# Performance work log

Measured on AMD Instinct MI355X. Metric: run time of the kernel, lower is better.

The kernel has to match this reference:

```python
import jax, jax.numpy as jnp
import numpy as np

EPS = 1e-4
MAX_LAPLACE_VAR = 1000.0
MAX_DENSITY = 10000.0
BINS = 256

_LAP_KERNEL = jnp.array([[0., 1., 0.], [1., -4., 1.], [0., 1., 0.]], dtype=jnp.float32)[None, None]  # OIHW [1,1,3,3]


def setup_inputs() -> dict:
    key = jax.random.key(0)
    k1, k2 = jax.random.split(key)
    rgb_img = jax.random.uniform(k1, (32, 3, 512, 512), dtype=jnp.float32)
    depth_img = jax.random.normal(k2, (32, 1, 512, 512), dtype=jnp.float32)
    return {"rgb_img": rgb_img, "depth_img": depth_img}


def _rgb_confidence(rgb_img):
    B, C, H, W = rgb_img.shape
    gray = 0.299 * rgb_img[:, 0] + 0.587 * rgb_img[:, 1] + 0.114 * rgb_img[:, 2]  # [B,H,W]
    gray = gray[:, None]  # [B,1,H,W]
    lap = jax.lax.conv_general_dilated(
        gray, _LAP_KERNEL, window_strides=(1, 1), padding=[(1, 1), (1, 1)],
        dimension_numbers=("NCHW", "OIHW", "NCHW"))
    # torch.var default is unbiased (ddof=1)
    laplace_var = jnp.var(lap, axis=(1, 2, 3), ddof=1)

    # integer-valued pixels 0..255 land exactly in histc bins 0..255 (bins=256, min=0, max=255)
    vals = jnp.clip(gray * 255.0, 0.0, 255.0).astype(jnp.int32)  # [B,1,H,W]
    vals = vals.reshape(B, -1)  # [B, H*W]
    bidx = jnp.broadcast_to(jnp.arange(B)[:, None], vals.shape)
    hist = jnp.zeros((B, BINS), jnp.float32).at[bidx, vals].add(1.0)
    p = hist / jnp.sum(hist, axis=1, keepdims=True)
    entropy = -jnp.sum(p * jnp.log2(p + EPS), axis=1)

    clarity_score = laplace_var / (MAX_LAPLACE_VAR + EPS)
    uniformity_score = 1.0 / (entropy + EPS)
    return (0.5 * (clarity_score + uniformity_score))[:, None]  # [B,1]


def _depth_confidence(depth_img):
    C = depth_img.shape[1]
    depth_map = depth_img[:, 2] if C == 3 else depth_img[:, 0]  # [B,H,W]
    mask = (depth_map > 0).astype(jnp.float32)
    density = jnp.mean(mask, axis=(1, 2))

    # vectorized masked std (unbiased, ddof=1), matching torch.std over valid pixels
    n = jnp.sum(mask, axis=(1, 2))  # [B]
    mean = jnp.sum(depth_map * mask, axis=(1, 2)) / jnp.maximum(n, 1.0)
    sq = jnp.sum(mask * (depth_map - mean[:, None, None]) ** 2, axis=(1, 2))
    var = sq / jnp.maximum(n - 1.0, 1.0)
    std = jnp.sqrt(jnp.maximum(var, 0.0))
    noise_level = jnp.where(n > 0, std, 1.0)

    density_score = density / (MAX_DENSITY + EPS)
    noise_score = 1.0 / (noise_level + EPS)
    return (0.5 * (density_score + noise_score))[:, None]  # [B,1]


def reference(rgb_img, depth_img):
    rgb_conf = _rgb_confidence(rgb_img)
    depth_conf = _depth_confidence(depth_img)
    denom = rgb_conf + depth_conf + EPS
    w_r = rgb_conf / denom
    w_d = depth_conf / denom
    return (w_r, w_d)
```

## Files before the change

### kernel.cpp

```cpp
#include <hip/hip_runtime.h>

#define IMG_H 512
#define IMG_W 512
#define HW (IMG_H * IMG_W)
#define NB 32
#define STRIPS 64
#define RPW 2

#define ACCP_DOUBLES (5 * NB * STRIPS)
#define HISTP_U32 (NB * STRIPS * 256)
#define WS_BYTES (ACCP_DOUBLES * 8 + HISTP_U32 * 4)

struct Row6 { float4 a0, a1, b0, b1, c0, c1; };

__device__ inline Row6 load_row(const float* __restrict__ rp, int r, int c0) {
    Row6 x;
    if ((unsigned)r < IMG_H) {
        const size_t o = (size_t)r * IMG_W + c0;
        x.a0 = *(const float4*)(rp + o);
        x.a1 = *(const float4*)(rp + o + 4);
        x.b0 = *(const float4*)(rp + HW + o);
        x.b1 = *(const float4*)(rp + HW + o + 4);
        x.c0 = *(const float4*)(rp + 2 * HW + o);
        x.c1 = *(const float4*)(rp + 2 * HW + o + 4);
    } else {
        const float4 z = {0.f, 0.f, 0.f, 0.f};
        x.a0 = x.a1 = x.b0 = x.b1 = x.c0 = x.c1 = z;
    }
    return x;
}

__device__ inline void to_gray(const Row6& x, float g[8]) {
    g[0] = 0.299f * x.a0.x + 0.587f * x.b0.x + 0.114f * x.c0.x;
    g[1] = 0.299f * x.a0.y + 0.587f * x.b0.y + 0.114f * x.c0.y;
    g[2] = 0.299f * x.a0.z + 0.587f * x.b0.z + 0.114f * x.c0.z;
    g[3] = 0.299f * x.a0.w + 0.587f * x.b0.w + 0.114f * x.c0.w;
    g[4] = 0.299f * x.a1.x + 0.587f * x.b1.x + 0.114f * x.c1.x;
    g[5] = 0.299f * x.a1.y + 0.587f * x.b1.y + 0.114f * x.c1.y;
    g[6] = 0.299f * x.a1.z + 0.587f * x.b1.z + 0.114f * x.c1.z;
    g[7] = 0.299f * x.a1.w + 0.587f * x.b1.w + 0.114f * x.c1.w;
}

__global__ __launch_bounds__(256, 2) void fused_kernel(
    const float* __restrict__ rgb, const float* __restrict__ depth,
    double* __restrict__ accp, unsigned int* __restrict__ histp)
{
    __shared__ unsigned int lh[4][256];
    __shared__ double red[4][5];

    const int t = threadIdx.x;
    const int b = blockIdx.y;
    const int x = blockIdx.x;
    const int s = ((x & 7) << 3) | (x >> 3);
    const int lane = t & 63;
    const int w = t >> 6;

    #pragma unroll
    for (int i = 0; i < 4; ++i) lh[i][t] = 0u;
    __syncthreads();

    const float* rp = rgb + (size_t)b * 3 * HW;
    const int rb = s * (4 * RPW) + w * RPW;
    const int c0 = lane * 8;

    const float4* dp = (const float4*)(depth + (size_t)b * HW + (size_t)s * (HW / STRIPS));

    Row6 r0 = load_row(rp, rb - 1, c0);
    Row6 r1 = load_row(rp, rb, c0);
    Row6 buf[2];
    float4 dv[2][2];
    buf[0] = load_row(rp, rb + 1, c0); dv[0][0] = dp[0 * 256 + t]; dv[0][1] = dp[1 * 256 + t];
    buf[1] = load_row(rp, rb + 2, c0); dv[1][0] = dp[2 * 256 + t]; dv[1][1] = dp[3 * 256 + t];

    float gp[8], gc[8], gn[8];
    to_gray(r0, gp);
    to_gray(r1, gc);

    float s1 = 0.f, s2 = 0.f;
    float dnf = 0.f, dsf = 0.f, dqf = 0.f;

    #pragma unroll
    for (int r = 0; r < RPW; ++r) {
        to_gray(buf[r], gn);
        const float4 d0 = dv[r][0];
        const float4 d1 = dv[r][1];

        float lf = __shfl_up(gc[7], 1, 64);
        if (lane == 0) lf = 0.f;
        float rt = __shfl_down(gc[0], 1, 64);
        if (lane == 63) rt = 0.f;

        #pragma unroll
        for (int j = 0; j < 8; ++j) {
            const float left  = (j == 0) ? lf : gc[j - 1];
            const float right = (j == 7) ? rt : gc[j + 1];
            const float lap = gp[j] + gn[j] + left + right - 4.f * gc[j];
            s1 += lap;
            s2 += lap * lap;
            atomicAdd(&lh[w][(int)fminf(fmaxf(gc[j] * 255.f, 0.f), 255.f)], 1u);
        }

        if (d0.x > 0.f) { dnf += 1.f; dsf += d0.x; dqf += d0.x * d0.x; }
        if (d0.y > 0.f) { dnf += 1.f; dsf += d0.y; dqf += d0.y * d0.y; }
        if (d0.z > 0.f) { dnf += 1.f; dsf += d0.z; dqf += d0.z * d0.z; }
        if (d0.w > 0.f) { dnf += 1.f; dsf += d0.w; dqf += d0.w * d0.w; }
        if (d1.x > 0.f) { dnf += 1.f; dsf += d1.x; dqf += d1.x * d1.x; }
        if (d1.y > 0.f) { dnf += 1.f; dsf += d1.y; dqf += d1.y * d1.y; }
        if (d1.z > 0.f) { dnf += 1.f; dsf += d1.z; dqf += d1.z * d1.z; }
        if (d1.w > 0.f) { dnf += 1.f; dsf += d1.w; dqf += d1.w * d1.w; }

        #pragma unroll
        for (int j = 0; j < 8; ++j) { gp[j] = gc[j]; gc[j] = gn[j]; }
    }

    double z0 = (double)s1, z1 = (double)s2, z2 = (double)dnf, z3 = (double)dsf, z4 = (double)dqf;
    for (int off = 32; off > 0; off >>= 1) {
        z0 += __shfl_down(z0, off, 64);
        z1 += __shfl_down(z1, off, 64);
        z2 += __shfl_down(z2, off, 64);
        z3 += __shfl_down(z3, off, 64);
        z4 += __shfl_down(z4, off, 64);
    }
    if (lane == 0) {
        red[w][0] = z0; red[w][1] = z1; red[w][2] = z2; red[w][3] = z3; red[w][4] = z4;
    }
    __syncthreads();

    const unsigned int hsum = lh[0][t] + lh[1][t] + lh[2][t] + lh[3][t];
    histp[((size_t)b * STRIPS + s) * 256 + t] = hsum;
    if (t < 5) {
        const double v = red[0][t] + red[1][t] + red[2][t] + red[3][t];
        accp[((size_t)t * NB + b) * STRIPS + s] = v;
    }
}

__global__ __launch_bounds__(256) void final_kernel(
    const double* __restrict__ accp,
    const unsigned int* __restrict__ histp,
    float* __restrict__ out)
{
    __shared__ float ent[4];
    __shared__ double sacc[5];

    const int t = threadIdx.x;
    const int b = blockIdx.x;
    const int lane = t & 63;
    const int w = t >> 6;

    unsigned int hv = 0u;
    #pragma unroll
    for (int s = 0; s < STRIPS; ++s)
        hv += histp[((size_t)b * STRIPS + s) * 256 + t];

    const float p = (float)hv * (1.0f / (float)HW);
    float term = p * log2f(p + 1e-4f);
    for (int off = 32; off > 0; off >>= 1) term += __shfl_down(term, off, 64);
    if (lane == 0) ent[w] = term;

    if (t < 160) {
        const int k = t >> 5, ss = t & 31;
        double v = accp[((size_t)k * NB + b) * STRIPS + ss]
                 + accp[((size_t)k * NB + b) * STRIPS + ss + 32];
        for (int off = 16; off > 0; off >>= 1) v += __shfl_down(v, off, 32);
        if (ss == 0) sacc[k] = v;
    }
    __syncthreads();

    if (t == 0) {
        const double entropy = -(double)(ent[0] + ent[1] + ent[2] + ent[3]);
        const double N = (double)HW;

        const double ls = sacc[0], lq = sacc[1];
        const double lvar = (lq - ls * ls / N) / (N - 1.0);
        const double clarity = lvar / (1000.0 + 1e-4);
        const double uniformity = 1.0 / (entropy + 1e-4);
        const double rgb_conf = 0.5 * (clarity + uniformity);

        const double n = sacc[2], sdep = sacc[3], q = sacc[4];
        const double mean = sdep / fmax(n, 1.0);
        const double sq = q - 2.0 * mean * sdep + mean * mean * n;
        const double var = sq / fmax(n - 1.0, 1.0);
        const double stdd = sqrt(fmax(var, 0.0));
        const double noise = (n > 0.0) ? stdd : 1.0;
        const double density = n / N;
        const double depth_conf = 0.5 * (density / (10000.0 + 1e-4) + 1.0 / (noise + 1e-4));

        const double denom = rgb_conf + depth_conf + 1e-4;
        out[b]      = (float)(rgb_conf / denom);
        out[NB + b] = (float)(depth_conf / denom);
    }
}

extern "C" void kernel_launch(void* const* d_in, const int* in_sizes, int n_in,
                              void* d_out, int out_size, void* d_ws, size_t ws_size,
                              hipStream_t stream) {
    const float* rgb   = (const float*)d_in[0];
    const float* depth = (const float*)d_in[1];
    float* out = (float*)d_out;

    double* accp = (double*)d_ws;
    unsigned int* histp = (unsigned int*)((char*)d_ws + ACCP_DOUBLES * 8);

    fused_kernel<<<dim3(STRIPS, NB), 256, 0, stream>>>(rgb, depth, accp, histp);
    final_kernel<<<NB, 256, 0, stream>>>(accp, histp, out);
}
```

Measured before the change: 173.6 us.

## Split rows into column halves with deeper per-warp row streaming

Each block now covers half the image width (4 floats per lane) over 4 rows per warp instead of full width over 2 rows. Halo columns at the split are fetched with scalar edge loads. Row loads are software-pipelined one row ahead instead of all up front, which cuts register pressure, and launch bounds rise to 4 blocks per CU for more occupancy. The cost is extra scalar edge loads and smaller 16-byte accesses per lane, and the previous strip swizzle is dropped.

```diff
diff --git a/kernel.cpp b/kernel.cpp
--- a/kernel.cpp
+++ b/kernel.cpp
@@ -4,44 +4,46 @@
 #define IMG_W 512
 #define HW (IMG_H * IMG_W)
 #define NB 32
-#define STRIPS 64
-#define RPW 2
-
-#define ACCP_DOUBLES (5 * NB * STRIPS)
-#define HISTP_U32 (NB * STRIPS * 256)
+#define NSX 64
+#define RPW 4
+#define DSLOT (HW / NSX)
+
+#define ACCP_DOUBLES (5 * NB * NSX)
+#define HISTP_U32 (NB * NSX * 256)
 #define WS_BYTES (ACCP_DOUBLES * 8 + HISTP_U32 * 4)
 
-struct Row6 { float4 a0, a1, b0, b1, c0, c1; };
-
-__device__ inline Row6 load_row(const float* __restrict__ rp, int r, int c0) {
-    Row6 x;
+struct RowH { float4 a, b, c; };
+
+__device__ inline RowH load_rowh(const float* __restrict__ rp, int r, int c0) {
+    RowH x;
     if ((unsigned)r < IMG_H) {
         const size_t o = (size_t)r * IMG_W + c0;
-        x.a0 = *(const float4*)(rp + o);
-        x.a1 = *(const float4*)(rp + o + 4);
-        x.b0 = *(const float4*)(rp + HW + o);
-        x.b1 = *(const float4*)(rp + HW + o + 4);
-        x.c0 = *(const float4*)(rp + 2 * HW + o);
-        x.c1 = *(const float4*)(rp + 2 * HW + o + 4);
+        x.a = *(const float4*)(rp + o);
+        x.b = *(const float4*)(rp + HW + o);
+        x.c = *(const float4*)(rp + 2 * HW + o);
     } else {
         const float4 z = {0.f, 0.f, 0.f, 0.f};
-        x.a0 = x.a1 = x.b0 = x.b1 = x.c0 = x.c1 = z;
+        x.a = x.b = x.c = z;
     }
     return x;
 }
 
-__device__ inline void to_gray(const Row6& x, float g[8]) {
-    g[0] = 0.299f * x.a0.x + 0.587f * x.b0.x + 0.114f * x.c0.x;
-    g[1] = 0.299f * x.a0.y + 0.587f * x.b0.y + 0.114f * x.c0.y;
-    g[2] = 0.299f * x.a0.z + 0.587f * x.b0.z + 0.114f * x.c0.z;
-    g[3] = 0.299f * x.a0.w + 0.587f * x.b0.w + 0.114f * x.c0.w;
-    g[4] = 0.299f * x.a1.x + 0.587f * x.b1.x + 0.114f * x.c1.x;
-    g[5] = 0.299f * x.a1.y + 0.587f * x.b1.y + 0.114f * x.c1.y;
-    g[6] = 0.299f * x.a1.z + 0.587f * x.b1.z + 0.114f * x.c1.z;
-    g[7] = 0.299f * x.a1.w + 0.587f * x.b1.w + 0.114f * x.c1.w;
-}
-
-__global__ __launch_bounds__(256, 2) void fused_kernel(
+__device__ inline void to_gray4(const RowH& x, float g[4]) {
+    g[0] = 0.299f * x.a.x + 0.587f * x.b.x + 0.114f * x.c.x;
+    g[1] = 0.299f * x.a.y + 0.587f * x.b.y + 0.114f * x.c.y;
+    g[2] = 0.299f * x.a.z + 0.587f * x.b.z + 0.114f * x.c.z;
+    g[3] = 0.299f * x.a.w + 0.587f * x.b.w + 0.114f * x.c.w;
+}
+
+__device__ inline float edge_gray(const float* __restrict__ rp, int r, int ecol) {
+    if ((unsigned)r < IMG_H) {
+        const size_t o = (size_t)r * IMG_W + ecol;
+        return 0.299f * rp[o] + 0.587f * rp[HW + o] + 0.114f * rp[2 * HW + o];
+    }
+    return 0.f;
+}
+
+__global__ __launch_bounds__(256, 4) void fused_kernel(
     const float* __restrict__ rgb, const float* __restrict__ depth,
     double* __restrict__ accp, unsigned int* __restrict__ histp)
 {
@@ -51,7 +53,8 @@
     const int t = threadIdx.x;
     const int b = blockIdx.y;
     const int x = blockIdx.x;
-    const int s = ((x & 7) << 3) | (x >> 3);
+    const int rs = x >> 1;
+    const int h  = x & 1;
     const int lane = t & 63;
     const int w = t >> 6;
 
@@ -60,57 +63,61 @@
     __syncthreads();
 
     const float* rp = rgb + (size_t)b * 3 * HW;
-    const int rb = s * (4 * RPW) + w * RPW;
-    const int c0 = lane * 8;
-
-    const float4* dp = (const float4*)(depth + (size_t)b * HW + (size_t)s * (HW / STRIPS));
-
-    Row6 r0 = load_row(rp, rb - 1, c0);
-    Row6 r1 = load_row(rp, rb, c0);
-    Row6 buf[2];
-    float4 dv[2][2];
-    buf[0] = load_row(rp, rb + 1, c0); dv[0][0] = dp[0 * 256 + t]; dv[0][1] = dp[1 * 256 + t];
-    buf[1] = load_row(rp, rb + 2, c0); dv[1][0] = dp[2 * 256 + t]; dv[1][1] = dp[3 * 256 + t];
-
-    float gp[8], gc[8], gn[8];
-    to_gray(r0, gp);
-    to_gray(r1, gc);
+    const int rb = rs * 16 + w * RPW;
+    const int c0 = h * 256 + lane * 4;
+    const int ecol = h ? 255 : 256;
+
+    const float4* dp = (const float4*)(depth + (size_t)b * HW + (size_t)x * DSLOT);
+
+    RowH r0 = load_rowh(rp, rb - 1, c0);
+    RowH r1 = load_rowh(rp, rb,     c0);
+    RowH stg = load_rowh(rp, rb + 1, c0);
+    float ec = edge_gray(rp, rb,     ecol);
+    float en = edge_gray(rp, rb + 1, ecol);
+    float4 dv[4];
+    #pragma unroll
+    for (int k = 0; k < 4; ++k) dv[k] = dp[k * 256 + t];
+
+    float gp[4], gc[4], gn[4];
+    to_gray4(r0, gp);
+    to_gray4(r1, gc);
 
     float s1 = 0.f, s2 = 0.f;
     float dnf = 0.f, dsf = 0.f, dqf = 0.f;
 
     #pragma unroll
     for (int r = 0; r < RPW; ++r) {
-        to_gray(buf[r], gn);
-        const float4 d0 = dv[r][0];
-        const float4 d1 = dv[r][1];
-
-        float lf = __shfl_up(gc[7], 1, 64);
-        if (lane == 0) lf = 0.f;
+        to_gray4(stg, gn);
+        float etmp = 0.f;
+        if (r < RPW - 1) {
+            stg = load_rowh(rp, rb + r + 2, c0);
+            etmp = edge_gray(rp, rb + r + 2, ecol);
+        }
+
+        float lf = __shfl_up(gc[3], 1, 64);
+        if (lane == 0)  lf = h ? ec : 0.f;
         float rt = __shfl_down(gc[0], 1, 64);
-        if (lane == 63) rt = 0.f;
+        if (lane == 63) rt = h ? 0.f : ec;
 
         #pragma unroll
-        for (int j = 0; j < 8; ++j) {
+        for (int j = 0; j < 4; ++j) {
             const float left  = (j == 0) ? lf : gc[j - 1];
-            const float right = (j == 7) ? rt : gc[j + 1];
+            const float right = (j == 3) ? rt : gc[j + 1];
             const float lap = gp[j] + gn[j] + left + right - 4.f * gc[j];
             s1 += lap;
             s2 += lap * lap;
             atomicAdd(&lh[w][(int)fminf(fmaxf(gc[j] * 255.f, 0.f), 255.f)], 1u);
         }
 
-        if (d0.x > 0.f) { dnf += 1.f; dsf += d0.x; dqf += d0.x * d0.x; }
-        if (d0.y > 0.f) { dnf += 1.f; dsf += d0.y; dqf += d0.y * d0.y; }
-        if (d0.z > 0.f) { dnf += 1.f; dsf += d0.z; dqf += d0.z * d0.z; }
-        if (d0.w > 0.f) { dnf += 1.f; dsf += d0.w; dqf += d0.w * d0.w; }
-        if (d1.x > 0.f) { dnf += 1.f; dsf += d1.x; dqf += d1.x * d1.x; }
-        if (d1.y > 0.f) { dnf += 1.f; dsf += d1.y; dqf += d1.y * d1.y; }
-        if (d1.z > 0.f) { dnf += 1.f; dsf += d1.z; dqf += d1.z * d1.z; }
-        if (d1.w > 0.f) { dnf += 1.f; dsf += d1.w; dqf += d1.w * d1.w; }
+        const float4 d = dv[r];
+        if (d.x > 0.f) { dnf += 1.f; dsf += d.x; dqf += d.x * d.x; }
+        if (d.y > 0.f) { dnf += 1.f; dsf += d.y; dqf += d.y * d.y; }
+        if (d.z > 0.f) { dnf += 1.f; dsf += d.z; dqf += d.z * d.z; }
+        if (d.w > 0.f) { dnf += 1.f; dsf += d.w; dqf += d.w * d.w; }
 
         #pragma unroll
-        for (int j = 0; j < 8; ++j) { gp[j] = gc[j]; gc[j] = gn[j]; }
+        for (int j = 0; j < 4; ++j) { gp[j] = gc[j]; gc[j] = gn[j]; }
+        ec = en; en = etmp;
     }
 
     double z0 = (double)s1, z1 = (double)s2, z2 = (double)dnf, z3 = (double)dsf, z4 = (double)dqf;
@@ -127,10 +134,10 @@
     __syncthreads();
 
     const unsigned int hsum = lh[0][t] + lh[1][t] + lh[2][t] + lh[3][t];
-    histp[((size_t)b * STRIPS + s) * 256 + t] = hsum;
+    histp[((size_t)b * NSX + x) * 256 + t] = hsum;
     if (t < 5) {
         const double v = red[0][t] + red[1][t] + red[2][t] + red[3][t];
-        accp[((size_t)t * NB + b) * STRIPS + s] = v;
+        accp[((size_t)t * NB + b) * NSX + x] = v;
     }
 }
 
@@ -149,8 +156,8 @@
 
     unsigned int hv = 0u;
     #pragma unroll
-    for (int s = 0; s < STRIPS; ++s)
-        hv += histp[((size_t)b * STRIPS + s) * 256 + t];
+    for (int s = 0; s < NSX; ++s)
+        hv += histp[((size_t)b * NSX + s) * 256 + t];
 
     const float p = (float)hv * (1.0f / (float)HW);
     float term = p * log2f(p + 1e-4f);
@@ -159,8 +166,8 @@
 
     if (t < 160) {
         const int k = t >> 5, ss = t & 31;
-        double v = accp[((size_t)k * NB + b) * STRIPS + ss]
-                 + accp[((size_t)k * NB + b) * STRIPS + ss + 32];
+        double v = accp[((size_t)k * NB + b) * NSX + ss]
+                 + accp[((size_t)k * NB + b) * NSX + ss + 32];
         for (int off = 16; off > 0; off >>= 1) v += __shfl_down(v, off, 32);
         if (ss == 0) sacc[k] = v;
     }
@@ -201,6 +208,6 @@
     double* accp = (double*)d_ws;
     unsigned int* histp = (unsigned int*)((char*)d_ws + ACCP_DOUBLES * 8);
 
-    fused_kernel<<<dim3(STRIPS, NB), 256, 0, stream>>>(rgb, depth, accp, histp);
+    fused_kernel<<<dim3(NSX, NB), 256, 0, stream>>>(rgb, depth, accp, histp);
     final_kernel<<<NB, 256, 0, stream>>>(accp, histp, out);
 }
```

Result: no change. 176.2 us (+1.5%).

## Share halo gray rows between waves via LDS instead of reloading them

Applied to the files above, without the earlier changes.

Each wave now loads only its own two rows, plus one halo row for the first and last waves. It converts them to gray and stores them in shared memory so neighbouring waves can read their halo rows from LDS. Before, every wave loaded four rows, so global RGB traffic per block drops from 16 row loads to 10. This adds 16KB of LDS and a barrier before compute, which could lower occupancy. Waves 0 and 3 also diverge on the extra loads.

```diff
diff --git a/kernel.cpp b/kernel.cpp
--- a/kernel.cpp
+++ b/kernel.cpp
@@ -45,6 +45,8 @@
     const float* __restrict__ rgb, const float* __restrict__ depth,
     double* __restrict__ accp, unsigned int* __restrict__ histp)
 {
+    __shared__ float gtop[4][512];
+    __shared__ float gbot[4][512];
     __shared__ unsigned int lh[4][256];
     __shared__ double red[4][5];
 
@@ -57,60 +59,91 @@
 
     #pragma unroll
     for (int i = 0; i < 4; ++i) lh[i][t] = 0u;
+
+    const float* rp = rgb + (size_t)b * 3 * HW;
+    const int rb = s * 8 + w * RPW;
+    const int c0 = lane * 8;
+
+    const float4* dp = (const float4*)(depth + (size_t)b * HW + (size_t)s * (HW / STRIPS));
+
+    Row6 rA = load_row(rp, rb,     c0);
+    Row6 rB = load_row(rp, rb + 1, c0);
+    Row6 rT, rD;
+    if (w == 0) rT = load_row(rp, rb - 1, c0);
+    if (w == 3) rD = load_row(rp, rb + 2, c0);
+    float4 dv[4];
+    #pragma unroll
+    for (int k = 0; k < 4; ++k) dv[k] = dp[k * 256 + t];
+
+    float ga[8], gb[8];
+    to_gray(rA, ga);
+    to_gray(rB, gb);
+    #pragma unroll
+    for (int j = 0; j < 8; ++j) { gtop[w][c0 + j] = ga[j]; gbot[w][c0 + j] = gb[j]; }
+
+    float gt[8], gd[8];
+    if (w == 0) to_gray(rT, gt);
+    if (w == 3) to_gray(rD, gd);
+
     __syncthreads();
 
-    const float* rp = rgb + (size_t)b * 3 * HW;
-    const int rb = s * (4 * RPW) + w * RPW;
-    const int c0 = lane * 8;
-
-    const float4* dp = (const float4*)(depth + (size_t)b * HW + (size_t)s * (HW / STRIPS));
-
-    Row6 r0 = load_row(rp, rb - 1, c0);
-    Row6 r1 = load_row(rp, rb, c0);
-    Row6 buf[2];
-    float4 dv[2][2];
-    buf[0] = load_row(rp, rb + 1, c0); dv[0][0] = dp[0 * 256 + t]; dv[0][1] = dp[1 * 256 + t];
-    buf[1] = load_row(rp, rb + 2, c0); dv[1][0] = dp[2 * 256 + t]; dv[1][1] = dp[3 * 256 + t];
-
-    float gp[8], gc[8], gn[8];
-    to_gray(r0, gp);
-    to_gray(r1, gc);
+    float ha[8], hb[8];
+    if (w == 0) {
+        #pragma unroll
+        for (int j = 0; j < 8; ++j) ha[j] = gt[j];
+    } else {
+        #pragma unroll
+        for (int j = 0; j < 8; ++j) ha[j] = gbot[w - 1][c0 + j];
+    }
+    if (w == 3) {
+        #pragma unroll
+        for (int j = 0; j < 8; ++j) hb[j] = gd[j];
+    } else {
+        #pragma unroll
+        for (int j = 0; j < 8; ++j) hb[j] = gtop[w + 1][c0 + j];
+    }
 
     float s1 = 0.f, s2 = 0.f;
     float dnf = 0.f, dsf = 0.f, dqf = 0.f;
 
-    #pragma unroll
-    for (int r = 0; r < RPW; ++r) {
-        to_gray(buf[r], gn);
-        const float4 d0 = dv[r][0];
-        const float4 d1 = dv[r][1];
-
-        float lf = __shfl_up(gc[7], 1, 64);
+    {
+        float lf = __shfl_up(ga[7], 1, 64);
         if (lane == 0) lf = 0.f;
-        float rt = __shfl_down(gc[0], 1, 64);
+        float rt = __shfl_down(ga[0], 1, 64);
         if (lane == 63) rt = 0.f;
-
         #pragma unroll
         for (int j = 0; j < 8; ++j) {
-            const float left  = (j == 0) ? lf : gc[j - 1];
-            const float right = (j == 7) ? rt : gc[j + 1];
-            const float lap = gp[j] + gn[j] + left + right - 4.f * gc[j];
+            const float left  = (j == 0) ? lf : ga[j - 1];
+            const float right = (j == 7) ? rt : ga[j + 1];
+            const float lap = ha[j] + gb[j] + left + right - 4.f * ga[j];
             s1 += lap;
             s2 += lap * lap;
-            atomicAdd(&lh[w][(int)fminf(fmaxf(gc[j] * 255.f, 0.f), 255.f)], 1u);
+            atomicAdd(&lh[w][(int)fminf(fmaxf(ga[j] * 255.f, 0.f), 255.f)], 1u);
         }
-
-        if (d0.x > 0.f) { dnf += 1.f; dsf += d0.x; dqf += d0.x * d0.x; }
-        if (d0.y > 0.f) { dnf += 1.f; dsf += d0.y; dqf += d0.y * d0.y; }
-        if (d0.z > 0.f) { dnf += 1.f; dsf += d0.z; dqf += d0.z * d0.z; }
-        if (d0.w > 0.f) { dnf += 1.f; dsf += d0.w; dqf += d0.w * d0.w; }
-        if (d1.x > 0.f) { dnf += 1.f; dsf += d1.x; dqf += d1.x * d1.x; }
-        if (d1.y > 0.f) { dnf += 1.f; dsf += d1.y; dqf += d1.y * d1.y; }
-        if (d1.z > 0.f) { dnf += 1.f; dsf += d1.z; dqf += d1.z * d1.z; }
-        if (d1.w > 0.f) { dnf += 1.f; dsf += d1.w; dqf += d1.w * d1.w; }
-
-        #pragma unroll
-        for (int j = 0; j < 8; ++j) { gp[j] = gc[j]; gc[j] = gn[j]; }
+    }
+    {
+        float lf = __shfl_up(gb[7], 1, 64);
+        if (lane == 0) lf = 0.f;
+        float rt = __shfl_down(gb[0], 1, 64);
+        if (lane == 63) rt = 0.f;
+        #pragma unroll
+        for (int j = 0; j < 8; ++j) {
+            const float left  = (j == 0) ? lf : gb[j - 1];
+            const float right = (j == 7) ? rt : gb[j + 1];
+            const float lap = ga[j] + hb[j] + left + right - 4.f * gb[j];
+            s1 += lap;
+            s2 += lap * lap;
+            atomicAdd(&lh[w][(int)fminf(fmaxf(gb[j] * 255.f, 0.f), 255.f)], 1u);
+        }
+    }
+
+    #pragma unroll
+    for (int k = 0; k < 4; ++k) {
+        const float4 d = dv[k];
+        if (d.x > 0.f) { dnf += 1.f; dsf += d.x; dqf += d.x * d.x; }
+        if (d.y > 0.f) { dnf += 1.f; dsf += d.y; dqf += d.y * d.y; }
+        if (d.z > 0.f) { dnf += 1.f; dsf += d.z; dqf += d.z * d.z; }
+        if (d.w > 0.f) { dnf += 1.f; dsf += d.w; dqf += d.w * d.w; }
     }
 
     double z0 = (double)s1, z1 = (double)s2, z2 = (double)dnf, z3 = (double)dsf, z4 = (double)dqf;
```

Result: no change. 172.6 us (-0.6%).
